# Performance work log

Measured on AMD Instinct MI355X. Metric: run time of the kernel, lower is better.

## Reference

```python
import jax, jax.numpy as jnp
import numpy as np

B, S, H, V, LLM_D, NL = 256, 200, 128, 50000, 768, 2
H2 = 2 * H
PAD_L = 256  # next power of two >= S
EPS = 1e-12


def _ln(x, g, b):
    mu = jnp.mean(x, axis=-1, keepdims=True)
    var = jnp.mean((x - mu) ** 2, axis=-1, keepdims=True)
    return (x - mu) / jnp.sqrt(var + EPS) * g + b


def _gelu(x):
    return jax.nn.gelu(x, approximate=False)


def _lru_scan(h, lamb0, mask):
    # Faithful recursive-doubling masked LRU scan.
    # h: [B, L, D] complex64; mask: [B, L] float32; lamb0: [1, D] complex64
    Bb, L, D = h.shape
    lamb = lamb0
    for i in range(1, int(np.log2(L)) + 1):
        l = 2 ** i
        h = h.reshape(Bb * L // l, l, D)
        m = mask.reshape(Bb * L // l, l)
        h1, h2 = h[:, : l // 2], h[:, l // 2 :]
        if i > 1:
            lamb = jnp.concatenate([lamb, lamb * lamb[-1]], axis=0)
        h2 = h2 + lamb * h1[:, -1:] * m[:, l // 2 - 1 : l // 2, None]
        h = jnp.concatenate([h1, h2], axis=1)
    return h.reshape(Bb, L, D)


def setup_inputs() -> dict:
    rng = np.random.default_rng(0)
    key = jax.random.key(0)
    ks = jax.random.split(key, 16)
    std = 0.02
    r_min, r_max = 0.8, 0.99
    # ring init of LRU diagonal (per layer)
    u1 = rng.uniform(size=(NL, H2)); u2 = rng.uniform(size=(NL, H2))
    nu_log = np.log(-0.5 * np.log(u1 * (r_max ** 2 - r_min ** 2) + r_min ** 2))
    theta_log = np.log(u2 * 2 * np.pi)
    diag = np.exp(-np.exp(nu_log) + 1j * np.exp(theta_log))
    gamma_log = np.log(np.sqrt(1 - np.abs(diag) ** 2))
    params_log = jnp.asarray(np.stack([nu_log, theta_log, gamma_log], axis=1), jnp.float32)  # [NL,3,H2]
    f32 = jnp.float32

    def rn(k, shape, s=std):
        return jax.random.normal(k, shape, f32) * s

    return dict(
        input_ids=jax.random.randint(ks[0], (B, S), 0, V),
        item_emb=rn(ks[1], (V, H)),
        llm_emb=rn(ks[2], (V, LLM_D), 1.0),
        W_map=rn(ks[3], (H, LLM_D)), b_map=jnp.zeros((H,), f32),
        Wg1=rn(ks[4], (2 * H, 2 * H)), bg1=jnp.zeros((2 * H,), f32),
        Wg2=rn(ks[5], (H, 2 * H)), bg2=jnp.zeros((H,), f32),
        ln0_g=jnp.ones((H,), f32), ln0_b=jnp.zeros((H,), f32),
        params_log=params_log,
        Win_re=rn(ks[6], (NL, H2, H)), Win_im=rn(ks[7], (NL, H2, H)),
        bin_re=jnp.zeros((NL, H2), f32), bin_im=jnp.zeros((NL, H2), f32),
        Wout_re=rn(ks[8], (NL, H, H2)), Wout_im=rn(ks[9], (NL, H, H2)),
        bout_re=jnp.zeros((NL, H), f32), bout_im=jnp.zeros((NL, H), f32),
        ln1_g=jnp.ones((NL, H), f32), ln1_b=jnp.zeros((NL, H), f32),
        Wff1=rn(ks[10], (NL, 4 * H, H)), bff1=jnp.zeros((NL, 4 * H), f32),
        Wff2=rn(ks[11], (NL, H, 4 * H)), bff2=jnp.zeros((NL, H), f32),
        ln2_g=jnp.ones((NL, H), f32), ln2_b=jnp.zeros((NL, H), f32),
    )


def reference(input_ids, item_emb, llm_emb, W_map, b_map, Wg1, bg1, Wg2, bg2,
              ln0_g, ln0_b, params_log, Win_re, Win_im, bin_re, bin_im,
              Wout_re, Wout_im, bout_re, bout_im, ln1_g, ln1_b,
              Wff1, bff1, Wff2, bff2, ln2_g, ln2_b):
    mask = input_ids > 0
    # dual embedding + dimension gating (dropout off in eval)
    ids = item_emb[input_ids]                              # [B,S,H]
    llm = llm_emb[input_ids] @ W_map.T + b_map             # [B,S,H]
    cat = jnp.concatenate([ids, llm], axis=-1)
    gate = jax.nn.sigmoid(_gelu(cat @ Wg1.T + bg1) @ Wg2.T + bg2)
    x = _ln(gate * ids + (1.0 - gate) * llm, ln0_g, ln0_b)
    pad = PAD_L - x.shape[1]
    x = jnp.pad(x, ((0, 0), (pad, 0), (0, 0)))             # left-pad seq dim
    m = jnp.pad(mask, ((0, 0), (pad, 0))).astype(jnp.float32)
    for l in range(NL):
        # --- LRU layer ---
        nu, theta, gamma = jnp.exp(params_log[l])          # each [H2]
        lamb0 = jnp.exp(-nu + 1j * theta)[None, :].astype(jnp.complex64)
        Win = (Win_re[l] + 1j * Win_im[l]).astype(jnp.complex64)
        bin_ = (bin_re[l] + 1j * bin_im[l]).astype(jnp.complex64)
        Wout = (Wout_re[l] + 1j * Wout_im[l]).astype(jnp.complex64)
        bout = (bout_re[l] + 1j * bout_im[l]).astype(jnp.complex64)
        h = (x.astype(jnp.complex64) @ Win.T + bin_) * gamma
        h = _lru_scan(h, lamb0, m)
        x = _ln((h @ Wout.T + bout).real + x, ln1_g[l], ln1_b[l])
        # --- position-wise FFN (Intermediate) ---
        ff = _gelu(x @ Wff1[l].T + bff1[l]) @ Wff2[l].T + bff2[l]
        x = _ln(ff + x, ln2_g[l], ln2_b[l])
    return x[:, -S:]
```

## Files before the change

### kernel.cpp

```cpp
#include <hip/hip_runtime.h>
#include <hip/hip_bf16.h>

#define CB 256
#define CS 200
#define CH 128
#define CH2 256
#define CL 256
#define CPAD 56
#define CBS (CB*CS)

typedef __attribute__((ext_vector_type(8))) short bf16x8;
typedef __attribute__((ext_vector_type(4))) float f32x4;

#define SB16 ((long)CBS*16)

__device__ __align__(16) __hip_bfloat16 g_cat [(size_t)CBS*256];
__device__ __align__(16) __hip_bfloat16 g_g1  [(size_t)CBS*256];
__device__ __align__(16) __hip_bfloat16 g_xb  [(size_t)CBS*128];
__device__ __align__(16) __hip_bfloat16 g_h   [(size_t)CBS*512];
__device__ __align__(16) __hip_bfloat16 g_ffh [(size_t)CBS*512];
__device__ float g_mask[CB*CL];
__device__ float g_gamma2[2*512];
__device__ float g_bincat[2*512];
__device__ float2 g_lam[2*16*128*16];
__device__ __align__(16) __hip_bfloat16 g_Wmap  [128*768];
__device__ __align__(16) __hip_bfloat16 g_Wg1   [256*256];
__device__ __align__(16) __hip_bfloat16 g_Wg2   [128*256];
__device__ __align__(16) __hip_bfloat16 g_Wincat[2*512*128];
__device__ __align__(16) __hip_bfloat16 g_Woutcat[2*128*512];
__device__ __align__(16) __hip_bfloat16 g_Wff1  [2*512*128];
__device__ __align__(16) __hip_bfloat16 g_Wff2  [2*128*512];

__device__ __forceinline__ short f2bf(float f){
  unsigned u = __float_as_uint(f);
  unsigned r = (u + 0x7fffu + ((u>>16)&1u)) >> 16;
  return (short)r;
}
__device__ __forceinline__ float bf2f(short s){
  return __uint_as_float(((unsigned)(unsigned short)s) << 16);
}

typedef const __attribute__((address_space(1))) void* gas1;
typedef __attribute__((address_space(3))) void* las3;
__device__ __forceinline__ void gl16(const void* g, void* l){
  __builtin_amdgcn_global_load_lds((gas1)g, (las3)l, 16, 0, 0);
}

__global__ void k_mask(const int* __restrict__ ids){
  int b = blockIdx.x, t = threadIdx.x;
  float m = 0.f;
  if (t >= CPAD) m = (ids[b*CS + (t - CPAD)] > 0) ? 1.f : 0.f;
  g_mask[b*CL + t] = m;
}

__global__ void k_gather_ids(const int* __restrict__ ids,
                             const float* __restrict__ item_emb){
  int tok = blockIdx.x, c = threadIdx.x;
  int id = ids[tok];
  ((short*)g_cat)[(long)(c>>4)*SB16 + (long)tok*16 + (c&15)]
      = f2bf(item_emb[(size_t)id*128 + c]);
}

__device__ __forceinline__ void wblk(__hip_bfloat16* dst, int N, int K, int i, float v){
  int r = i / K, c = i - r*K;
  ((short*)dst)[(long)(c>>4)*((long)N*16) + (long)r*16 + (c&15)] = f2bf(v);
}
__global__ void k_wcvt_all(const float* __restrict__ W_map, const float* __restrict__ Wg1,
                           const float* __restrict__ Wg2,
                           const float* __restrict__ Win_re, const float* __restrict__ Win_im,
                           const float* __restrict__ Wout_re, const float* __restrict__ Wout_im,
                           const float* __restrict__ Wff1, const float* __restrict__ Wff2){
  int i = blockIdx.x*256 + threadIdx.x;
  if (i < 98304){ wblk(g_Wmap, 128, 768, i, W_map[i]); return; }
  i -= 98304;
  if (i < 65536){ wblk(g_Wg1, 256, 256, i, Wg1[i]); return; }
  i -= 65536;
  if (i < 32768){ wblk(g_Wg2, 128, 256, i, Wg2[i]); return; }
  i -= 32768;
  int l = i / 262144; i -= l*262144;
  if (i < 32768){ wblk(g_Wincat + (long)l*65536, 512, 128, i,       Win_re[(long)l*32768 + i]); return; }
  i -= 32768;
  if (i < 32768){ wblk(g_Wincat + (long)l*65536, 512, 128, i+32768, Win_im[(long)l*32768 + i]); return; }
  i -= 32768;
  if (i < 65536){
    int r = i >> 9, c = i & 511;
    float v = (c < 256) ? Wout_re[(long)l*32768 + r*256 + c]
                        : -Wout_im[(long)l*32768 + r*256 + (c-256)];
    wblk(g_Woutcat + (long)l*65536, 128, 512, i, v); return;
  }
  i -= 65536;
  if (i < 65536){ wblk(g_Wff1 + (long)l*65536, 512, 128, i, Wff1[(long)l*65536 + i]); return; }
  i -= 65536;
  wblk(g_Wff2 + (long)l*65536, 128, 512, i, Wff2[(long)l*65536 + i]);
}

__global__ void k_prep(const float* __restrict__ pl,
                       const float* __restrict__ binre,
                       const float* __restrict__ binim){
  int l = blockIdx.x, d = threadIdx.x;
  float nu = expf(pl[(l*3+0)*CH2 + d]);
  float th = expf(pl[(l*3+1)*CH2 + d]);
  float gm = expf(pl[(l*3+2)*CH2 + d]);
  g_gamma2[l*512 + d] = gm;       g_gamma2[l*512 + d + 256] = gm;
  g_bincat[l*512 + d] = binre[l*256 + d];
  g_bincat[l*512 + d + 256] = binim[l*256 + d];
  float r = expf(-nu);
  float lre = r*cosf(th), lim = r*sinf(th);
  float pr = lre, pi = lim;
  long base = ((long)l*16 + (d>>4))*2048 + (d&15);
  for (int k = 0; k < 128; k++){
    g_lam[base + (long)k*16] = make_float2(pr, pi);
    float nr = pr*lre - pi*lim;
    float ni = pr*lim + pi*lre;
    pr = nr; pi = ni;
  }
}

template<int ACT, int EPI, bool GATHER, bool COLSCALE>
__device__ __forceinline__ void mgemm_body(
    const short* __restrict__ A, const float* __restrict__ Af32, int ldaF,
    const short* __restrict__ W, long wBlkStride,
    const float* __restrict__ bias, const float* __restrict__ gamma,
    const int* __restrict__ gidx, short* __restrict__ C,
    long aBlkStride, int colOff, int K,
    const float* __restrict__ lnG, const float* __restrict__ lnB)
{
  __shared__ __align__(16) char lA[16384];
  __shared__ __align__(16) char lB[16384];
  constexpr int MF = (EPI==0)?4:2;
  constexpr int NF = (EPI==0)?4:8;
  const int t = threadIdx.x;
  const int m0 = blockIdx.x*128, n0 = blockIdx.y*128;
  const int lane = t & 63, wv = t >> 6;
  const int wr = (EPI==0)?(wv>>1):wv;
  const int wc = (EPI==0)?(wv&1):0;
  const int fr = lane & 15, fq = lane >> 4;
  const int rowB = wr*(MF*16), colB = wc*64;

  long gr = 0;
  if (GATHER) gr = gidx[m0 + (t>>1)];

  f32x4 acc[MF][NF] = {};

  for (int k0 = 0; k0 < K; k0 += 64){
    if (GATHER){
      int row = t>>1, half = t&1;
      #pragma unroll
      for (int cc = 0; cc < 4; cc++){
        const float* p = Af32 + gr*(long)ldaF + k0 + cc*16 + half*8;
        float4 x0 = *(const float4*)p;
        float4 x1 = *(const float4*)(p + 4);
        bf16x8 v;
        v[0]=f2bf(x0.x); v[1]=f2bf(x0.y); v[2]=f2bf(x0.z); v[3]=f2bf(x0.w);
        v[4]=f2bf(x1.x); v[5]=f2bf(x1.y); v[6]=f2bf(x1.z); v[7]=f2bf(x1.w);
        *(bf16x8*)(lA + cc*4096 + row*32 + half*16) = v;
      }
    } else {
      #pragma unroll
      for (int cc = 0; cc < 4; cc++){
        const short* gp = A + (long)((k0>>4)+cc)*aBlkStride + (long)(m0 + wv*32)*16 + (lane<<3);
        gl16(gp, lA + cc*4096 + wv*1024);
      }
    }
    #pragma unroll
    for (int cc = 0; cc < 4; cc++){
      const short* gp = W + (long)((k0>>4)+cc)*wBlkStride + (long)(n0 + wv*32)*16 + (lane<<3);
      gl16(gp, lB + cc*4096 + wv*1024);
    }
    __syncthreads();
    #pragma unroll
    for (int s = 0; s < 2; s++){
      bf16x8 af[MF], bw[NF];
      #pragma unroll
      for (int m = 0; m < MF; m++)
        af[m] = *(const bf16x8*)(lA + (s*2+(fq>>1))*4096 + (rowB + m*16 + fr)*32 + (fq&1)*16);
      #pragma unroll
      for (int n = 0; n < NF; n++)
        bw[n] = *(const bf16x8*)(lB + (s*2+(fq>>1))*4096 + (colB + n*16 + fr)*32 + (fq&1)*16);
      #pragma unroll
      for (int m = 0; m < MF; m++)
        #pragma unroll
        for (int n = 0; n < NF; n++)
          acc[m][n] = __builtin_amdgcn_mfma_f32_16x16x32_bf16(af[m], bw[n], acc[m][n], 0, 0, 0);
    }
    __syncthreads();
  }

  if (EPI == 0){
    #pragma unroll
    for (int m = 0; m < MF; m++){
      #pragma unroll
      for (int j = 0; j < 4; j++){
        long row = m0 + rowB + m*16 + fq*4 + j;
        #pragma unroll
        for (int n = 0; n < NF; n++){
          int colL = n0 + colB + n*16 + fr;
          float v = acc[m][n][j] + bias[colL];
          if (COLSCALE) v *= gamma[colL];
          if (ACT == 1) v = 0.5f * v * (1.0f + erff(v * 0.70710678118654752f));
          int colS = colL + colOff;
          C[(long)(colS>>4)*SB16 + row*16 + (colS&15)] = f2bf(v);
        }
      }
    }
  } else {
    #pragma unroll
    for (int m = 0; m < MF; m++){
      #pragma unroll
      for (int j = 0; j < 4; j++){
        int rt = rowB + m*16 + fq*4 + j;
        long tok = m0 + rt;
        float vv[NF];
        float s1 = 0.f, s2 = 0.f;
        #pragma unroll
        for (int n = 0; n < NF; n++){
          int col = n*16 + fr;
          float v = acc[m][n][j] + bias[col];
          if (EPI == 2){
            v = 1.0f / (1.0f + expf(-v));
            float idv = bf2f(((const short*)g_cat)[(long)n*SB16 + tok*16 + fr]);
            float lmv = bf2f(((const short*)g_cat)[(long)(n+8)*SB16 + tok*16 + fr]);
            v = v*idv + (1.0f - v)*lmv;
          } else {
            v += bf2f(((const short*)g_xb)[(long)n*SB16 + tok*16 + fr]);
          }
          vv[n] = v; s1 += v; s2 += v*v;
        }
        #pragma unroll
        for (int off = 1; off < 16; off <<= 1){
          s1 += __shfl_xor(s1, off); s2 += __shfl_xor(s2, off);
        }
        float mu = s1 * (1.f/128.f);
        float var = s2 * (1.f/128.f) - mu*mu;
        float rstd = rsqrtf(var + 1e-12f);
        #pragma unroll
        for (int n = 0; n < NF; n++){
          int col = n*16 + fr;
          float o = (vv[n] - mu)*rstd*lnG[col] + lnB[col];
          ((short*)g_xb)[(long)n*SB16 + tok*16 + fr] = f2bf(o);
        }
      }
    }
  }
}

__global__ __launch_bounds__(256) void kg_llm(const float* llm_emb, const float* b_map, const int* ids){
  mgemm_body<0,0,true,false>(nullptr, llm_emb, 768, (const short*)g_Wmap, 128L*16,
                             b_map, nullptr, ids, (short*)g_cat, 0, 128, 768, nullptr, nullptr);
}
__global__ __launch_bounds__(256) void kg_g1(const float* bg1){
  mgemm_body<1,0,false,false>((const short*)g_cat, nullptr, 0, (const short*)g_Wg1, 256L*16,
                              bg1, nullptr, nullptr, (short*)g_g1, SB16, 0, 256, nullptr, nullptr);
}
__global__ __launch_bounds__(256) void kg_gate(const float* bg2, const float* ln0g, const float* ln0b){
  mgemm_body<0,2,false,false>((const short*)g_g1, nullptr, 0, (const short*)g_Wg2, 128L*16,
                              bg2, nullptr, nullptr, nullptr, SB16, 0, 256, ln0g, ln0b);
}
__global__ __launch_bounds__(256) void kg_h(int l){
  mgemm_body<0,0,false,true>((const short*)g_xb, nullptr, 0,
                             (const short*)g_Wincat + (long)l*65536, 512L*16,
                             g_bincat + l*512, g_gamma2 + l*512, nullptr, (short*)g_h,
                             SB16, 0, 128, nullptr, nullptr);
}
__global__ __launch_bounds__(256) void kg_out(int l, const float* bout, const float* g, const float* b){
  mgemm_body<0,1,false,false>((const short*)g_h, nullptr, 0,
                              (const short*)g_Woutcat + (long)l*65536, 128L*16,
                              bout, nullptr, nullptr, nullptr, SB16, 0, 512, g, b);
}
__global__ __launch_bounds__(256) void kg_ff1(int l, const float* bff1){
  mgemm_body<1,0,false,false>((const short*)g_xb, nullptr, 0,
                              (const short*)g_Wff1 + (long)l*65536, 512L*16,
                              bff1, nullptr, nullptr, (short*)g_ffh, SB16, 0, 128, nullptr, nullptr);
}
__global__ __launch_bounds__(256) void kg_ff2(int l, const float* bff2, const float* g, const float* b){
  mgemm_body<0,1,false,false>((const short*)g_ffh, nullptr, 0,
                              (const short*)g_Wff2 + (long)l*65536, 128L*16,
                              bff2, nullptr, nullptr, nullptr, SB16, 0, 512, g, b);
}

__global__ __launch_bounds__(256) void k_scan(int l){
  __shared__ __align__(16) float sre[CL*16];
  __shared__ __align__(16) float sim[CL*16];
  __shared__ float smask[CL];
  int b = blockIdx.y, ch = blockIdx.x;
  int tid = threadIdx.x;
  short* Hre = (short*)g_h + (long)ch*SB16 + (long)b*CS*16;
  short* Him = (short*)g_h + (long)(ch+16)*SB16 + (long)b*CS*16;
  smask[tid] = g_mask[b*CL + tid];
  for (int q = tid; q < 224; q += 256){
    ((float4*)sre)[q] = make_float4(0.f,0.f,0.f,0.f);
    ((float4*)sim)[q] = make_float4(0.f,0.f,0.f,0.f);
  }
  for (int q = tid; q < 400; q += 256){
    bf16x8 r8 = ((const bf16x8*)Hre)[q];
    bf16x8 i8 = ((const bf16x8*)Him)[q];
    int base = 896 + q*8;
    #pragma unroll
    for (int k = 0; k < 8; k++){ sre[base+k] = bf2f(r8[k]); sim[base+k] = bf2f(i8[k]); }
  }
  __syncthreads();
  const float2* lam = g_lam + ((long)l*16 + ch)*2048;
  const int dl = tid & 15, u0 = tid >> 4;
  for (int i = 1; i <= 8; i++){
    int hl = 1 << (i-1);
    #pragma unroll
    for (int k = 0; k < 8; k++){
      int u = u0 + k*16;
      int blkI = u >> (i-1), j = u & (hl-1);
      int p = (blkI << i) + hl - 1;
      int tt = p + 1 + j;
      float mv = smask[p];
      float2 L = lam[j*16 + dl];
      float hr = sre[p*16+dl], hi = sim[p*16+dl];
      sre[tt*16+dl] += (L.x*hr - L.y*hi) * mv;
      sim[tt*16+dl] += (L.x*hi + L.y*hr) * mv;
    }
    __syncthreads();
  }
  for (int q = tid; q < 400; q += 256){
    int base = 896 + q*8;
    bf16x8 r8, i8;
    #pragma unroll
    for (int k = 0; k < 8; k++){ r8[k] = f2bf(sre[base+k]); i8[k] = f2bf(sim[base+k]); }
    ((bf16x8*)Hre)[q] = r8;
    ((bf16x8*)Him)[q] = i8;
  }
}

__global__ void k_copy_out(float* __restrict__ out){
  int i = blockIdx.x*256 + threadIdx.x;
  int tok = i >> 7, c = i & (CH-1);
  out[i] = bf2f(((const short*)g_xb)[(long)(c>>4)*SB16 + (long)tok*16 + (c&15)]);
}

extern "C" void kernel_launch(void* const* d_in, const int* in_sizes, int n_in,
                              void* d_out, int out_size, void* d_ws, size_t ws_size,
                              hipStream_t stream) {
  const int*   ids       = (const int*)  d_in[0];
  const float* item_emb  = (const float*)d_in[1];
  const float* llm_emb   = (const float*)d_in[2];
  const float* W_map     = (const float*)d_in[3];
  const float* b_map     = (const float*)d_in[4];
  const float* Wg1       = (const float*)d_in[5];
  const float* bg1       = (const float*)d_in[6];
  const float* Wg2       = (const float*)d_in[7];
  const float* bg2       = (const float*)d_in[8];
  const float* ln0_g     = (const float*)d_in[9];
  const float* ln0_b     = (const float*)d_in[10];
  const float* params_log= (const float*)d_in[11];
  const float* Win_re    = (const float*)d_in[12];
  const float* Win_im    = (const float*)d_in[13];
  const float* bin_re    = (const float*)d_in[14];
  const float* bin_im    = (const float*)d_in[15];
  const float* Wout_re   = (const float*)d_in[16];
  const float* Wout_im   = (const float*)d_in[17];
  const float* bout_re   = (const float*)d_in[18];
  const float* ln1_g     = (const float*)d_in[20];
  const float* ln1_b     = (const float*)d_in[21];
  const float* Wff1      = (const float*)d_in[22];
  const float* bff1      = (const float*)d_in[23];
  const float* Wff2      = (const float*)d_in[24];
  const float* bff2      = (const float*)d_in[25];
  const float* ln2_g     = (const float*)d_in[26];
  const float* ln2_b     = (const float*)d_in[27];
  float* out = (float*)d_out;

  dim3 blk(256);

  k_wcvt_all<<<2816, blk, 0, stream>>>(W_map, Wg1, Wg2, Win_re, Win_im,
                                       Wout_re, Wout_im, Wff1, Wff2);
  k_prep<<<2, 256, 0, stream>>>(params_log, bin_re, bin_im);
  k_mask<<<CB, CL, 0, stream>>>(ids);
  k_gather_ids<<<CBS, CH, 0, stream>>>(ids, item_emb);

  kg_llm<<<dim3(400,1), blk, 0, stream>>>(llm_emb, b_map, ids);
  kg_g1 <<<dim3(400,2), blk, 0, stream>>>(bg1);
  kg_gate<<<dim3(400,1), blk, 0, stream>>>(bg2, ln0_g, ln0_b);

  for (int l = 0; l < 2; l++){
    kg_h  <<<dim3(400,4), blk, 0, stream>>>(l);
    k_scan<<<dim3(16,CB), blk, 0, stream>>>(l);
    kg_out<<<dim3(400,1), blk, 0, stream>>>(l, bout_re + l*128, ln1_g + l*128, ln1_b + l*128);
    kg_ff1<<<dim3(400,4), blk, 0, stream>>>(l, bff1 + l*512);
    kg_ff2<<<dim3(400,1), blk, 0, stream>>>(l, bff2 + l*128, ln2_g + l*128, ln2_b + l*128);
  }

  k_copy_out<<<(CBS*CH)/256, blk, 0, stream>>>(out);
}
```

Measured before the change: 440.3 us.

## Halve GEMM M-tile for narrow GEMMs, merge setup kernels, vectorize gather and copy-out

```diff
diff --git a/kernel.cpp b/kernel.cpp
--- a/kernel.cpp
+++ b/kernel.cpp
@@ -46,137 +46,166 @@
   __builtin_amdgcn_global_load_lds((gas1)g, (las3)l, 16, 0, 0);
 }
 
-__global__ void k_mask(const int* __restrict__ ids){
-  int b = blockIdx.x, t = threadIdx.x;
-  float m = 0.f;
-  if (t >= CPAD) m = (ids[b*CS + (t - CPAD)] > 0) ? 1.f : 0.f;
-  g_mask[b*CL + t] = m;
-}
-
-__global__ void k_gather_ids(const int* __restrict__ ids,
-                             const float* __restrict__ item_emb){
-  int tok = blockIdx.x, c = threadIdx.x;
-  int id = ids[tok];
-  ((short*)g_cat)[(long)(c>>4)*SB16 + (long)tok*16 + (c&15)]
-      = f2bf(item_emb[(size_t)id*128 + c]);
-}
-
 __device__ __forceinline__ void wblk(__hip_bfloat16* dst, int N, int K, int i, float v){
   int r = i / K, c = i - r*K;
   ((short*)dst)[(long)(c>>4)*((long)N*16) + (long)r*16 + (c&15)] = f2bf(v);
 }
-__global__ void k_wcvt_all(const float* __restrict__ W_map, const float* __restrict__ Wg1,
-                           const float* __restrict__ Wg2,
-                           const float* __restrict__ Win_re, const float* __restrict__ Win_im,
-                           const float* __restrict__ Wout_re, const float* __restrict__ Wout_im,
-                           const float* __restrict__ Wff1, const float* __restrict__ Wff2){
-  int i = blockIdx.x*256 + threadIdx.x;
-  if (i < 98304){ wblk(g_Wmap, 128, 768, i, W_map[i]); return; }
-  i -= 98304;
-  if (i < 65536){ wblk(g_Wg1, 256, 256, i, Wg1[i]); return; }
-  i -= 65536;
-  if (i < 32768){ wblk(g_Wg2, 128, 256, i, Wg2[i]); return; }
-  i -= 32768;
-  int l = i / 262144; i -= l*262144;
-  if (i < 32768){ wblk(g_Wincat + (long)l*65536, 512, 128, i,       Win_re[(long)l*32768 + i]); return; }
-  i -= 32768;
-  if (i < 32768){ wblk(g_Wincat + (long)l*65536, 512, 128, i+32768, Win_im[(long)l*32768 + i]); return; }
-  i -= 32768;
-  if (i < 65536){
-    int r = i >> 9, c = i & 511;
-    float v = (c < 256) ? Wout_re[(long)l*32768 + r*256 + c]
-                        : -Wout_im[(long)l*32768 + r*256 + (c-256)];
-    wblk(g_Woutcat + (long)l*65536, 128, 512, i, v); return;
-  }
-  i -= 65536;
-  if (i < 65536){ wblk(g_Wff1 + (long)l*65536, 512, 128, i, Wff1[(long)l*65536 + i]); return; }
-  i -= 65536;
-  wblk(g_Wff2 + (long)l*65536, 128, 512, i, Wff2[(long)l*65536 + i]);
-}
-
-__global__ void k_prep(const float* __restrict__ pl,
-                       const float* __restrict__ binre,
-                       const float* __restrict__ binim){
-  int l = blockIdx.x, d = threadIdx.x;
-  float nu = expf(pl[(l*3+0)*CH2 + d]);
-  float th = expf(pl[(l*3+1)*CH2 + d]);
-  float gm = expf(pl[(l*3+2)*CH2 + d]);
-  g_gamma2[l*512 + d] = gm;       g_gamma2[l*512 + d + 256] = gm;
-  g_bincat[l*512 + d] = binre[l*256 + d];
-  g_bincat[l*512 + d + 256] = binim[l*256 + d];
-  float r = expf(-nu);
-  float lre = r*cosf(th), lim = r*sinf(th);
-  float pr = lre, pi = lim;
-  long base = ((long)l*16 + (d>>4))*2048 + (d&15);
-  for (int k = 0; k < 128; k++){
-    g_lam[base + (long)k*16] = make_float2(pr, pi);
-    float nr = pr*lre - pi*lim;
-    float ni = pr*lim + pi*lre;
-    pr = nr; pi = ni;
-  }
-}
-
-template<int ACT, int EPI, bool GATHER, bool COLSCALE>
+__global__ void k_setup(const float* __restrict__ W_map, const float* __restrict__ Wg1,
+                        const float* __restrict__ Wg2,
+                        const float* __restrict__ Win_re, const float* __restrict__ Win_im,
+                        const float* __restrict__ Wout_re, const float* __restrict__ Wout_im,
+                        const float* __restrict__ Wff1, const float* __restrict__ Wff2,
+                        const int* __restrict__ ids,
+                        const float* __restrict__ pl,
+                        const float* __restrict__ binre, const float* __restrict__ binim){
+  int bi = blockIdx.x, t = threadIdx.x;
+  if (bi < 2816){
+    int i = bi*256 + t;
+    if (i < 98304){ wblk(g_Wmap, 128, 768, i, W_map[i]); return; }
+    i -= 98304;
+    if (i < 65536){ wblk(g_Wg1, 256, 256, i, Wg1[i]); return; }
+    i -= 65536;
+    if (i < 32768){ wblk(g_Wg2, 128, 256, i, Wg2[i]); return; }
+    i -= 32768;
+    int l = i / 262144; i -= l*262144;
+    if (i < 32768){ wblk(g_Wincat + (long)l*65536, 512, 128, i,       Win_re[(long)l*32768 + i]); return; }
+    i -= 32768;
+    if (i < 32768){ wblk(g_Wincat + (long)l*65536, 512, 128, i+32768, Win_im[(long)l*32768 + i]); return; }
+    i -= 32768;
+    if (i < 65536){
+      int r = i >> 9, c = i & 511;
+      float v = (c < 256) ? Wout_re[(long)l*32768 + r*256 + c]
+                          : -Wout_im[(long)l*32768 + r*256 + (c-256)];
+      wblk(g_Woutcat + (long)l*65536, 128, 512, i, v); return;
+    }
+    i -= 65536;
+    if (i < 65536){ wblk(g_Wff1 + (long)l*65536, 512, 128, i, Wff1[(long)l*65536 + i]); return; }
+    i -= 65536;
+    wblk(g_Wff2 + (long)l*65536, 128, 512, i, Wff2[(long)l*65536 + i]);
+    return;
+  }
+  if (bi < 3072){
+    int b = bi - 2816;
+    float m = 0.f;
+    if (t >= CPAD) m = (ids[b*CS + (t - CPAD)] > 0) ? 1.f : 0.f;
+    g_mask[b*CL + t] = m;
+    return;
+  }
+  {
+    int l = bi - 3072, d = t;
+    float nu = expf(pl[(l*3+0)*CH2 + d]);
+    float th = expf(pl[(l*3+1)*CH2 + d]);
+    float gm = expf(pl[(l*3+2)*CH2 + d]);
+    g_gamma2[l*512 + d] = gm;       g_gamma2[l*512 + d + 256] = gm;
+    g_bincat[l*512 + d] = binre[l*256 + d];
+    g_bincat[l*512 + d + 256] = binim[l*256 + d];
+    float r = expf(-nu);
+    float lre = r*cosf(th), lim = r*sinf(th);
+    float pr = lre, pi = lim;
+    long base = ((long)l*16 + (d>>4))*2048 + (d&15);
+    for (int k = 0; k < 128; k++){
+      g_lam[base + (long)k*16] = make_float2(pr, pi);
+      float nr = pr*lre - pi*lim;
+      float ni = pr*lim + pi*lre;
+      pr = nr; pi = ni;
+    }
+  }
+}
+
+__global__ __launch_bounds__(256) void k_gather_ids(const int* __restrict__ ids,
+                                                    const float* __restrict__ item_emb){
+  int t = threadIdx.x;
+  int tok = blockIdx.x*16 + (t>>4);
+  int cg = t & 15;
+  int id = ids[tok];
+  const float* p = item_emb + (size_t)id*128 + cg*8;
+  float4 x0 = *(const float4*)p;
+  float4 x1 = *(const float4*)(p + 4);
+  bf16x8 v;
+  v[0]=f2bf(x0.x); v[1]=f2bf(x0.y); v[2]=f2bf(x0.z); v[3]=f2bf(x0.w);
+  v[4]=f2bf(x1.x); v[5]=f2bf(x1.y); v[6]=f2bf(x1.z); v[7]=f2bf(x1.w);
+  *(bf16x8*)((short*)g_cat + (long)(cg>>1)*SB16 + (long)tok*16 + (cg&1)*8) = v;
+}
+
+template<int TM, int ACT, int EPI, bool GATHER, bool COLSCALE>
 __device__ __forceinline__ void mgemm_body(
     const short* __restrict__ A, const float* __restrict__ Af32, int ldaF,
-    const short* __restrict__ W, long wBlkStride,
+    const short* __restrict__ W, long wBlk,
     const float* __restrict__ bias, const float* __restrict__ gamma,
     const int* __restrict__ gidx, short* __restrict__ C,
-    long aBlkStride, int colOff, int K,
+    long aBlk, int colOff, int K,
     const float* __restrict__ lnG, const float* __restrict__ lnB)
 {
-  __shared__ __align__(16) char lA[16384];
+  constexpr int ACH = TM*32;
+  __shared__ __align__(16) char lA[TM*128];
   __shared__ __align__(16) char lB[16384];
-  constexpr int MF = (EPI==0)?4:2;
-  constexpr int NF = (EPI==0)?4:8;
+  constexpr int MF = (EPI==0) ? (TM/32) : 1;
+  constexpr int NF = (EPI==0) ? 4 : 8;
   const int t = threadIdx.x;
-  const int m0 = blockIdx.x*128, n0 = blockIdx.y*128;
+  const int m0 = blockIdx.x*TM, n0 = blockIdx.y*128;
   const int lane = t & 63, wv = t >> 6;
   const int wr = (EPI==0)?(wv>>1):wv;
   const int wc = (EPI==0)?(wv&1):0;
   const int fr = lane & 15, fq = lane >> 4;
-  const int rowB = wr*(MF*16), colB = wc*64;
-
-  long gr = 0;
-  if (GATHER) gr = gidx[m0 + (t>>1)];
+  const int rowB = (EPI==0) ? wr*(TM/2) : wv*16;
+  const int colB = wc*64;
+
+  long gr0 = 0, gr1 = 0;
+  if (GATHER){ gr0 = gidx[m0 + (t>>3)]; gr1 = gidx[m0 + (t>>3) + 32]; }
 
   f32x4 acc[MF][NF] = {};
 
   for (int k0 = 0; k0 < K; k0 += 64){
-    if (GATHER){
-      int row = t>>1, half = t&1;
+    if (TM == 128){
       #pragma unroll
       for (int cc = 0; cc < 4; cc++){
-        const float* p = Af32 + gr*(long)ldaF + k0 + cc*16 + half*8;
-        float4 x0 = *(const float4*)p;
-        float4 x1 = *(const float4*)(p + 4);
-        bf16x8 v;
-        v[0]=f2bf(x0.x); v[1]=f2bf(x0.y); v[2]=f2bf(x0.z); v[3]=f2bf(x0.w);
-        v[4]=f2bf(x1.x); v[5]=f2bf(x1.y); v[6]=f2bf(x1.z); v[7]=f2bf(x1.w);
-        *(bf16x8*)(lA + cc*4096 + row*32 + half*16) = v;
+        const short* gp = A + (long)((k0>>4)+cc)*aBlk + (long)(m0 + wv*32)*16 + (lane<<3);
+        gl16(gp, lA + cc*4096 + wv*1024);
+      }
+      #pragma unroll
+      for (int cc = 0; cc < 4; cc++){
+        const short* gp = W + (long)((k0>>4)+cc)*wBlk + (long)(n0 + wv*32)*16 + (lane<<3);
+        gl16(gp, lB + cc*4096 + wv*1024);
       }
     } else {
-      #pragma unroll
-      for (int cc = 0; cc < 4; cc++){
-        const short* gp = A + (long)((k0>>4)+cc)*aBlkStride + (long)(m0 + wv*32)*16 + (lane<<3);
-        gl16(gp, lA + cc*4096 + wv*1024);
-      }
-    }
-    #pragma unroll
-    for (int cc = 0; cc < 4; cc++){
-      const short* gp = W + (long)((k0>>4)+cc)*wBlkStride + (long)(n0 + wv*32)*16 + (lane<<3);
-      gl16(gp, lB + cc*4096 + wv*1024);
+      if (GATHER){
+        #pragma unroll
+        for (int rep = 0; rep < 2; rep++){
+          int slot = t + rep*256;
+          int row = slot>>3, cc = (slot>>1)&3, half = slot&1;
+          long ar = rep ? gr1 : gr0;
+          const float* p = Af32 + ar*(long)ldaF + k0 + cc*16 + half*8;
+          float4 x0 = *(const float4*)p;
+          float4 x1 = *(const float4*)(p + 4);
+          bf16x8 v;
+          v[0]=f2bf(x0.x); v[1]=f2bf(x0.y); v[2]=f2bf(x0.z); v[3]=f2bf(x0.w);
+          v[4]=f2bf(x1.x); v[5]=f2bf(x1.y); v[6]=f2bf(x1.z); v[7]=f2bf(x1.w);
+          *(bf16x8*)(lA + cc*2048 + row*32 + half*16) = v;
+        }
+      } else {
+        #pragma unroll
+        for (int p = 0; p < 2; p++){
+          const short* gp = A + (long)((k0>>4)+wv)*aBlk + (long)(m0 + p*32 + (lane>>1))*16 + (lane&1)*8;
+          gl16(gp, lA + wv*2048 + p*1024);
+        }
+      }
+      #pragma unroll
+      for (int p = 0; p < 4; p++){
+        const short* gp = W + (long)((k0>>4)+wv)*wBlk + (long)(n0 + p*32 + (lane>>1))*16 + (lane&1)*8;
+        gl16(gp, lB + wv*4096 + p*1024);
+      }
     }
     __syncthreads();
     #pragma unroll
     for (int s = 0; s < 2; s++){
+      const int cc = s*2 + (fq>>1);
       bf16x8 af[MF], bw[NF];
       #pragma unroll
       for (int m = 0; m < MF; m++)
-        af[m] = *(const bf16x8*)(lA + (s*2+(fq>>1))*4096 + (rowB + m*16 + fr)*32 + (fq&1)*16);
+        af[m] = *(const bf16x8*)(lA + cc*ACH + (rowB + m*16 + fr)*32 + (fq&1)*16);
       #pragma unroll
       for (int n = 0; n < NF; n++)
-        bw[n] = *(const bf16x8*)(lB + (s*2+(fq>>1))*4096 + (colB + n*16 + fr)*32 + (fq&1)*16);
+        bw[n] = *(const bf16x8*)(lB + cc*4096 + (colB + n*16 + fr)*32 + (fq&1)*16);
       #pragma unroll
       for (int m = 0; m < MF; m++)
         #pragma unroll
@@ -205,77 +234,74 @@
     }
   } else {
     #pragma unroll
-    for (int m = 0; m < MF; m++){
-      #pragma unroll
-      for (int j = 0; j < 4; j++){
-        int rt = rowB + m*16 + fq*4 + j;
-        long tok = m0 + rt;
-        float vv[NF];
-        float s1 = 0.f, s2 = 0.f;
-        #pragma unroll
-        for (int n = 0; n < NF; n++){
-          int col = n*16 + fr;
-          float v = acc[m][n][j] + bias[col];
-          if (EPI == 2){
-            v = 1.0f / (1.0f + expf(-v));
-            float idv = bf2f(((const short*)g_cat)[(long)n*SB16 + tok*16 + fr]);
-            float lmv = bf2f(((const short*)g_cat)[(long)(n+8)*SB16 + tok*16 + fr]);
-            v = v*idv + (1.0f - v)*lmv;
-          } else {
-            v += bf2f(((const short*)g_xb)[(long)n*SB16 + tok*16 + fr]);
-          }
-          vv[n] = v; s1 += v; s2 += v*v;
+    for (int j = 0; j < 4; j++){
+      int rt = rowB + fq*4 + j;
+      long tok = m0 + rt;
+      float vv[NF];
+      float s1 = 0.f, s2 = 0.f;
+      #pragma unroll
+      for (int n = 0; n < NF; n++){
+        int col = n*16 + fr;
+        float v = acc[0][n][j] + bias[col];
+        if (EPI == 2){
+          v = 1.0f / (1.0f + expf(-v));
+          float idv = bf2f(((const short*)g_cat)[(long)n*SB16 + tok*16 + fr]);
+          float lmv = bf2f(((const short*)g_cat)[(long)(n+8)*SB16 + tok*16 + fr]);
+          v = v*idv + (1.0f - v)*lmv;
+        } else {
+          v += bf2f(((const short*)g_xb)[(long)n*SB16 + tok*16 + fr]);
         }
-        #pragma unroll
-        for (int off = 1; off < 16; off <<= 1){
-          s1 += __shfl_xor(s1, off); s2 += __shfl_xor(s2, off);
-        }
-        float mu = s1 * (1.f/128.f);
-        float var = s2 * (1.f/128.f) - mu*mu;
-        float rstd = rsqrtf(var + 1e-12f);
-        #pragma unroll
-        for (int n = 0; n < NF; n++){
-          int col = n*16 + fr;
-          float o = (vv[n] - mu)*rstd*lnG[col] + lnB[col];
-          ((short*)g_xb)[(long)n*SB16 + tok*16 + fr] = f2bf(o);
-        }
+        vv[n] = v; s1 += v; s2 += v*v;
+      }
+      #pragma unroll
+      for (int off = 1; off < 16; off <<= 1){
+        s1 += __shfl_xor(s1, off); s2 += __shfl_xor(s2, off);
+      }
+      float mu = s1 * (1.f/128.f);
+      float var = s2 * (1.f/128.f) - mu*mu;
+      float rstd = rsqrtf(var + 1e-12f);
+      #pragma unroll
+      for (int n = 0; n < NF; n++){
+        int col = n*16 + fr;
+        float o = (vv[n] - mu)*rstd*lnG[col] + lnB[col];
+        ((short*)g_xb)[(long)n*SB16 + tok*16 + fr] = f2bf(o);
       }
     }
   }
 }
 
 __global__ __launch_bounds__(256) void kg_llm(const float* llm_emb, const float* b_map, const int* ids){
-  mgemm_body<0,0,true,false>(nullptr, llm_emb, 768, (const short*)g_Wmap, 128L*16,
-                             b_map, nullptr, ids, (short*)g_cat, 0, 128, 768, nullptr, nullptr);
+  mgemm_body<64,0,0,true,false>(nullptr, llm_emb, 768, (const short*)g_Wmap, 128L*16,
+                                b_map, nullptr, ids, (short*)g_cat, 0, 128, 768, nullptr, nullptr);
 }
 __global__ __launch_bounds__(256) void kg_g1(const float* bg1){
-  mgemm_body<1,0,false,false>((const short*)g_cat, nullptr, 0, (const short*)g_Wg1, 256L*16,
-                              bg1, nullptr, nullptr, (short*)g_g1, SB16, 0, 256, nullptr, nullptr);
+  mgemm_body<64,1,0,false,false>((const short*)g_cat, nullptr, 0, (const short*)g_Wg1, 256L*16,
+                                 bg1, nullptr, nullptr, (short*)g_g1, SB16, 0, 256, nullptr, nullptr);
 }
 __global__ __launch_bounds__(256) void kg_gate(const float* bg2, const float* ln0g, const float* ln0b){
-  mgemm_body<0,2,false,false>((const short*)g_g1, nullptr, 0, (const short*)g_Wg2, 128L*16,
-                              bg2, nullptr, nullptr, nullptr, SB16, 0, 256, ln0g, ln0b);
+  mgemm_body<64,0,2,false,false>((const short*)g_g1, nullptr, 0, (const short*)g_Wg2, 128L*16,
+                                 bg2, nullptr, nullptr, nullptr, SB16, 0, 256, ln0g, ln0b);
 }
 __global__ __launch_bounds__(256) void kg_h(int l){
-  mgemm_body<0,0,false,true>((const short*)g_xb, nullptr, 0,
-                             (const short*)g_Wincat + (long)l*65536, 512L*16,
-                             g_bincat + l*512, g_gamma2 + l*512, nullptr, (short*)g_h,
-                             SB16, 0, 128, nullptr, nullptr);
+  mgemm_body<128,0,0,false,true>((const short*)g_xb, nullptr, 0,
+                                 (const short*)g_Wincat + (long)l*65536, 512L*16,
+                                 g_bincat + l*512, g_gamma2 + l*512, nullptr, (short*)g_h,
+                                 SB16, 0, 128, nullptr, nullptr);
 }
 __global__ __launch_bounds__(256) void kg_out(int l, const float* bout, const float* g, const float* b){
-  mgemm_body<0,1,false,false>((const short*)g_h, nullptr, 0,
-                              (const short*)g_Woutcat + (long)l*65536, 128L*16,
-                              bout, nullptr, nullptr, nullptr, SB16, 0, 512, g, b);
+  mgemm_body<64,0,1,false,false>((const short*)g_h, nullptr, 0,
+                                 (const short*)g_Woutcat + (long)l*65536, 128L*16,
+                                 bout, nullptr, nullptr, nullptr, SB16, 0, 512, g, b);
 }
 __global__ __launch_bounds__(256) void kg_ff1(int l, const float* bff1){
-  mgemm_body<1,0,false,false>((const short*)g_xb, nullptr, 0,
-                              (const short*)g_Wff1 + (long)l*65536, 512L*16,
-                              bff1, nullptr, nullptr, (short*)g_ffh, SB16, 0, 128, nullptr, nullptr);
+  mgemm_body<128,1,0,false,false>((const short*)g_xb, nullptr, 0,
+                                  (const short*)g_Wff1 + (long)l*65536, 512L*16,
+                                  bff1, nullptr, nullptr, (short*)g_ffh, SB16, 0, 128, nullptr, nullptr);
 }
 __global__ __launch_bounds__(256) void kg_ff2(int l, const float* bff2, const float* g, const float* b){
-  mgemm_body<0,1,false,false>((const short*)g_ffh, nullptr, 0,
-                              (const short*)g_Wff2 + (long)l*65536, 128L*16,
-                              bff2, nullptr, nullptr, nullptr, SB16, 0, 512, g, b);
+  mgemm_body<64,0,1,false,false>((const short*)g_ffh, nullptr, 0,
+                                 (const short*)g_Wff2 + (long)l*65536, 128L*16,
+                                 bff2, nullptr, nullptr, nullptr, SB16, 0, 512, g, b);
 }
 
 __global__ __launch_bounds__(256) void k_scan(int l){
@@ -327,10 +353,12 @@
   }
 }
 
-__global__ void k_copy_out(float* __restrict__ out){
+__global__ __launch_bounds__(256) void k_copy_out(float* __restrict__ out){
   int i = blockIdx.x*256 + threadIdx.x;
-  int tok = i >> 7, c = i & (CH-1);
-  out[i] = bf2f(((const short*)g_xb)[(long)(c>>4)*SB16 + (long)tok*16 + (c&15)]);
+  int base = i*4;
+  int tok = base >> 7, c = base & 127;
+  short4 s4 = *(const short4*)((const short*)g_xb + (long)(c>>4)*SB16 + (long)tok*16 + (c&15));
+  *(float4*)(out + base) = make_float4(bf2f(s4.x), bf2f(s4.y), bf2f(s4.z), bf2f(s4.w));
 }
 
 extern "C" void kernel_launch(void* const* d_in, const int* in_sizes, int n_in,
@@ -367,23 +395,22 @@
 
   dim3 blk(256);
 
-  k_wcvt_all<<<2816, blk, 0, stream>>>(W_map, Wg1, Wg2, Win_re, Win_im,
-                                       Wout_re, Wout_im, Wff1, Wff2);
-  k_prep<<<2, 256, 0, stream>>>(params_log, bin_re, bin_im);
-  k_mask<<<CB, CL, 0, stream>>>(ids);
-  k_gather_ids<<<CBS, CH, 0, stream>>>(ids, item_emb);
-
-  kg_llm<<<dim3(400,1), blk, 0, stream>>>(llm_emb, b_map, ids);
-  kg_g1 <<<dim3(400,2), blk, 0, stream>>>(bg1);
-  kg_gate<<<dim3(400,1), blk, 0, stream>>>(bg2, ln0_g, ln0_b);
+  k_setup<<<3074, blk, 0, stream>>>(W_map, Wg1, Wg2, Win_re, Win_im,
+                                    Wout_re, Wout_im, Wff1, Wff2,
+                                    ids, params_log, bin_re, bin_im);
+  k_gather_ids<<<CBS/16, blk, 0, stream>>>(ids, item_emb);
+
+  kg_llm <<<dim3(800,1), blk, 0, stream>>>(llm_emb, b_map, ids);
+  kg_g1  <<<dim3(800,2), blk, 0, stream>>>(bg1);
+  kg_gate<<<dim3(800,1), blk, 0, stream>>>(bg2, ln0_g, ln0_b);
 
   for (int l = 0; l < 2; l++){
     kg_h  <<<dim3(400,4), blk, 0, stream>>>(l);
     k_scan<<<dim3(16,CB), blk, 0, stream>>>(l);
-    kg_out<<<dim3(400,1), blk, 0, stream>>>(l, bout_re + l*128, ln1_g + l*128, ln1_b + l*128);
+    kg_out<<<dim3(800,1), blk, 0, stream>>>(l, bout_re + l*128, ln1_g + l*128, ln1_b + l*128);
     kg_ff1<<<dim3(400,4), blk, 0, stream>>>(l, bff1 + l*512);
-    kg_ff2<<<dim3(400,1), blk, 0, stream>>>(l, bff2 + l*128, ln2_g + l*128, ln2_b + l*128);
-  }
-
-  k_copy_out<<<(CBS*CH)/256, blk, 0, stream>>>(out);
-}
+    kg_ff2<<<dim3(800,1), blk, 0, stream>>>(l, bff2 + l*128, ln2_g + l*128, ln2_b + l*128);
+  }
+
+  k_copy_out<<<(CBS*CH)/1024, blk, 0, stream>>>(out);
+}
```

Result: no change. 440.2 us (-0.0%).
